# Kernel optimization log

Hardware: AMD Instinct MI355X
Metric: run time of the kernel (lower is better)

Reference implementation:

```python
import jax, jax.numpy as jnp
import numpy as np

HEADS = 8

def setup_inputs() -> dict:
    key = jax.random.key(0)
    ks = jax.random.split(key, 10)
    B, C, D, W, H = 4, 256, 12, 12, 12
    dk = C // HEADS
    return {
        "x": jax.random.normal(ks[0], (B, C, D, W, H), jnp.float32),
        "wq": jax.random.normal(ks[1], (C, C), jnp.float32) * 0.05,
        "bq": jax.random.normal(ks[2], (C,), jnp.float32) * 0.05,
        "wk": jax.random.normal(ks[3], (C, C), jnp.float32) * 0.05,
        "bk": jax.random.normal(ks[4], (C,), jnp.float32) * 0.05,
        "wv": jax.random.normal(ks[5], (C, C), jnp.float32) * 0.05,
        "bv": jax.random.normal(ks[6], (C,), jnp.float32) * 0.05,
        "rel_d": jax.random.normal(ks[7], (1, HEADS, dk, D, 1, 1), jnp.float32),
        "rel_h": jax.random.normal(ks[8], (1, HEADS, dk, 1, 1, H), jnp.float32),
        "rel_w": jax.random.normal(ks[9], (1, HEADS, dk, 1, W, 1), jnp.float32),
    }


def reference(x, wq, bq, wk, bk, wv, bv, rel_d, rel_h, rel_w):
    B, C, D, W, H = x.shape
    dk = C // HEADS
    N = D * W * H

    def proj(w, b):
        # Conv3d kernel_size=1 == per-voxel linear over channels
        y = jnp.einsum('bcdwh,oc->bodwh', x, w) + b[None, :, None, None, None]
        return y.reshape(B, HEADS, dk, N)  # [B,h,dk,N]

    q = proj(wq, bq)
    k = proj(wk, bk)
    v = proj(wv, bv)

    # content-content: q^T k -> [B,h,N,N]
    cc = jnp.einsum('bhdn,bhdm->bhnm', q, k)
    # relative-position bias: (rel_h+rel_w+rel_d) broadcasts to [1,h,dk,D,W,H]
    pos = (rel_h + rel_w + rel_d).reshape(1, HEADS, dk, N)
    # content-position: pos^T @ q -> [B,h,N,N]
    cp = jnp.einsum('bhdn,bhdm->bhnm', pos, q)

    attn = jax.nn.softmax(cc + cp, axis=-1)  # [B,h,N,N]
    # out = v @ attn^T -> [B,h,dk,N]
    out = jnp.einsum('bhdn,bhmn->bhdm', v, attn)
    return out.reshape(B, C, D, W, H)
```

## Files before the change

### kernel.cpp

```cpp
#include <hip/hip_runtime.h>
#include <math.h>

#define HEADS 8
#define DK 32
#define B_ 4
#define C_ 256
#define NVOX 1728
#define DE 64
#define XPITCH 136
#define CPITCH 36
#define LOG2E 1.44269504088896f
#define JSPLIT 2
#define ITILES 14

typedef _Float16 f16x8 __attribute__((ext_vector_type(8)));
typedef __fp16 fp16x2 __attribute__((ext_vector_type(2)));
typedef float f32x16 __attribute__((ext_vector_type(16)));

__device__ inline float h2f(short s) {
    _Float16 h = *(_Float16*)&s;
    return (float)h;
}
__device__ inline f32x16 mfma32h(f16x8 a, f16x8 b, f32x16 c) {
    return __builtin_amdgcn_mfma_f32_32x32x16_f16(a, b, c, 0, 0, 0);
}
__device__ __forceinline__ void gl_lds16(const short* g, short* l) {
    __builtin_amdgcn_global_load_lds(
        (const __attribute__((address_space(1))) unsigned int*)g,
        (__attribute__((address_space(3))) unsigned int*)l, 16, 0, 0);
}

union H8 { _Float16 h[8]; uint4 v; };
union H4 { _Float16 h[4]; uint2 v; };
union PW { fp16x2 h2; unsigned int u; };

__global__ __launch_bounds__(256)
void prep_kernel(const float* __restrict__ x,
                 const float* __restrict__ wq, const float* __restrict__ wk,
                 const float* __restrict__ wv,
                 const float* __restrict__ rel_d, const float* __restrict__ rel_h,
                 const float* __restrict__ rel_w,
                 short* __restrict__ wf, short* __restrict__ xf,
                 short* __restrict__ Qf) {
    __shared__ float tile[64][65];
    int bid = blockIdx.x;
    int t = threadIdx.x;

    if (bid < 192) {
        int idx = (bid * 256 + t) * 4;
        int m = idx >> 16;
        const float* w = (m == 0) ? wq : (m == 1) ? wk : wv;
        float4 v = *(const float4*)&w[idx & 65535];
        H4 hh;
        hh.h[0] = (_Float16)v.x; hh.h[1] = (_Float16)v.y;
        hh.h[2] = (_Float16)v.z; hh.h[3] = (_Float16)v.w;
        *(uint2*)&wf[idx] = hh.v;
    } else if (bid < 624) {
        int q = bid - 192;
        int nb = (q % 27) * 64;
        int c0 = ((q / 27) % 4) * 64;
        int b  = q / 108;
        const float* xb = x + (size_t)b * C_ * NVOX;
        for (int e = t; e < 4096; e += 256) {
            int ci = e >> 6, nl = e & 63;
            tile[ci][nl] = xb[(size_t)(c0 + ci) * NVOX + nb + nl];
        }
        __syncthreads();
        for (int e = t; e < 512; e += 256) {
            int n = e >> 3, cg = (e & 7) * 8;
            H8 hi;
            #pragma unroll
            for (int j = 0; j < 8; j++) hi.h[j] = (_Float16)tile[cg + j][n];
            *(uint4*)&xf[((size_t)b * NVOX + nb + n) * C_ + c0 + cg] = hi.v;
        }
    } else {
        int q = bid - 624;
        int nb = (q % 27) * 64;
        int h  = (q / 27) % 8;
        int b  = q / 216;
        int bh = b * HEADS + h;
        int nl = t & 63, dd0 = (t >> 6) * 8;
        int n = nb + nl;
        int di = n / 144, wi = (n / 12) % 12, hi = n % 12;
        H8 ph;
        #pragma unroll
        for (int o = 0; o < 8; o++) {
            int hd = h * DK + dd0 + o;
            ph.h[o] = (_Float16)(rel_d[hd * 12 + di] + rel_w[hd * 12 + wi] +
                                 rel_h[hd * 12 + hi]);
        }
        *(uint4*)&Qf[((size_t)bh * NVOX + n) * DE + DK + dd0] = ph.v;
    }
}

struct FS {
    union {
        short xs[64 * XPITCH];
        float cbuf[3][64][CPITCH];
    } u;
};

__global__ __launch_bounds__(384, 4)
void fproj_kernel(const short* __restrict__ xf, const short* __restrict__ wf,
                  const float* __restrict__ bq, const float* __restrict__ bk,
                  const float* __restrict__ bv,
                  short* __restrict__ Qf, short* __restrict__ Kf,
                  short* __restrict__ Vf) {
    __shared__ FS sm;
    int nb = blockIdx.x * 64, h = blockIdx.y, b = blockIdx.z;
    int bh = b * HEADS + h;
    int t = threadIdx.x;
    int w = t >> 6, l = t & 63, ln = l & 31, hv = l >> 5;
    int mat = w >> 1, nh = w & 1;

    const short* xb = xf + ((size_t)b * NVOX + nb) * C_;
    const short* wA = wf + ((size_t)mat * C_ + h * DK + ln) * C_;
    int xrow = (nh * 32 + ln) * XPITCH;

    f32x16 acc;
    #pragma unroll
    for (int r = 0; r < 16; r++) acc[r] = 0.f;

    #pragma unroll 1
    for (int ch = 0; ch < 2; ch++) {
        __syncthreads();
        for (int e = t; e < 1024; e += 384) {
            int row = e >> 4, c8 = (e & 15) * 8;
            *(uint4*)&sm.u.xs[row * XPITCH + c8] =
                *(const uint4*)&xb[row * C_ + ch * 128 + c8];
        }
        __syncthreads();
        #pragma unroll 4
        for (int ks = 0; ks < 8; ks++) {
            int kl_ = ks * 16 + hv * 8;
            f16x8 a = *(const f16x8*)&wA[ch * 128 + kl_];
            f16x8 bfr = *(const f16x8*)&sm.u.xs[xrow + kl_];
            acc = mfma32h(a, bfr, acc);
        }
    }
    __syncthreads();

    const float* bias = (mat == 0) ? bq : (mat == 1) ? bk : bv;
    int ncol = nh * 32 + ln;
    #pragma unroll
    for (int q2 = 0; q2 < 4; q2++) {
        float4 cv;
        float* cvp = (float*)&cv;
        #pragma unroll
        for (int m = 0; m < 4; m++) {
            int o_loc = 8 * q2 + 4 * hv + m;
            cvp[m] = acc[4 * q2 + m] + bias[h * DK + o_loc];
        }
        *(float4*)&sm.u.cbuf[mat][ncol][8 * q2 + 4 * hv] = cv;
    }
    __syncthreads();

    if (t < 256) {
        int n = t >> 2, ddg = (t & 3) * 8;
        H8 qh, kh;
        #pragma unroll
        for (int j = 0; j < 8; j++) {
            qh.h[j] = (_Float16)sm.u.cbuf[0][n][ddg + j];
            kh.h[j] = (_Float16)sm.u.cbuf[1][n][ddg + j];
        }
        *(uint4*)&Qf[((size_t)bh * NVOX + nb + n) * DE + ddg] = qh.v;
        *(uint4*)&Kf[((size_t)bh * NVOX + nb + n) * DK + ddg] = kh.v;
    }
    if (t < 256) {
        int d = t >> 3, ng = (t & 7) * 8;
        H8 vv;
        #pragma unroll
        for (int j = 0; j < 8; j++)
            vv.h[j] = (_Float16)sm.u.cbuf[2][ng + j][d];
        *(uint4*)&Vf[((size_t)bh * DK + d) * NVOX + nb + ng] = vv.v;
    }
}

__global__ __launch_bounds__(256, 4)
void attn_kernel(const short* __restrict__ Qf, const short* __restrict__ Kf,
                 const short* __restrict__ Vf,
                 short* __restrict__ wsO, float* __restrict__ wsM,
                 float* __restrict__ wsL) {
    __shared__ __align__(16) short Ksm[2][4096];
    __shared__ __align__(16) short Vsm[2][2048];
    int id = blockIdx.x;
    int x8 = id & 7;
    int rr = id >> 3;
    int g  = rr / 28;
    int k_ = rr - g * 28;
    int bh = g * 8 + x8;
    int it = k_ >> 1;
    int jp = k_ & 1;
    int cnt = 14 - jp;
    int t = threadIdx.x;
    int w  = t >> 6;
    int l  = t & 63;
    int ln = l & 31;
    int hv = l >> 5;
    int i_glob = it * 128 + w * 32 + ln;
    int iq = i_glob < NVOX ? i_glob : NVOX - 1;

    const short* Qp = Qf + (size_t)bh * NVOX * DE;
    const short* Kp = Kf + (size_t)bh * NVOX * DK;
    const short* Vp = Vf + (size_t)bh * DK * NVOX;

    f16x8 qf[4];
    #pragma unroll
    for (int ks = 0; ks < 4; ks++)
        qf[ks] = *(const f16x8*)&Qp[(size_t)iq * DE + ks * 16 + hv * 8];

    int jb0 = jp * 14 * 64;

    const short* gk0 = Kp + (size_t)(jb0 + (l ^ (w + 0))) * DK + (w + 0) * 8;
    const short* gk1 = Qp + (size_t)(jb0 + (l ^ (w + 4))) * DE + (w + 0) * 8;
    int vb0 = 2 * w + hv;
    const short* gv0 = Vp + (size_t)(ln ^ vb0) * NVOX + jb0 + vb0 * 8;

#define STAGE(bufp) do {                                   \
        short* kl_ = &Ksm[bufp][0];                        \
        short* vl_ = &Vsm[bufp][0];                        \
        gl_lds16(gk0, kl_ + (w + 0) * 512);                \
        gl_lds16(gk1, kl_ + (w + 4) * 512);                \
        gl_lds16(gv0, vl_ + (w + 0) * 512);                \
        gk0 += 64 * DK; gk1 += 64 * DE; gv0 += 64;         \
    } while (0)

    float mL = -INFINITY;
    float lsum = 0.f;
    f32x16 O;
    #pragma unroll
    for (int r = 0; r < 16; r++) O[r] = 0.f;

    STAGE(0);

    #pragma unroll 1
    for (int jt = 0; jt < cnt; ++jt) {
        int buf = jt & 1;
        __syncthreads();
        if (jt + 1 < cnt) STAGE(buf ^ 1);

        const short* Kb = &Ksm[buf][0];
        const short* Vb = &Vsm[buf][0];

        f32x16 sc[2];
        __builtin_amdgcn_s_setprio(1);
        #pragma unroll
        for (int js = 0; js < 2; js++) {
            f32x16 s;
            #pragma unroll
            for (int r = 0; r < 16; r++) s[r] = 0.f;
            #pragma unroll
            for (int ks = 0; ks < 4; ks++) {
                int kb = ks * 2 + hv;
                f16x8 kfr = *(const f16x8*)&Kb[kb * 512 + js * 256 + (ln ^ kb) * 8];
                s = mfma32h(kfr, qf[ks], s);
            }
            sc[js] = s;
        }
        __builtin_amdgcn_s_setprio(0);

        float m0 = fmaxf(sc[0][0], sc[1][0]);
        float m1 = fmaxf(sc[0][1], sc[1][1]);
        float m2 = fmaxf(sc[0][2], sc[1][2]);
        float m3 = fmaxf(sc[0][3], sc[1][3]);
        #pragma unroll
        for (int r = 4; r < 16; r += 4) {
            m0 = fmaxf(m0, fmaxf(sc[0][r + 0], sc[1][r + 0]));
            m1 = fmaxf(m1, fmaxf(sc[0][r + 1], sc[1][r + 1]));
            m2 = fmaxf(m2, fmaxf(sc[0][r + 2], sc[1][r + 2]));
            m3 = fmaxf(m3, fmaxf(sc[0][r + 3], sc[1][r + 3]));
        }
        float mx = fmaxf(fmaxf(m0, m1), fmaxf(m2, m3));
        mx = fmaxf(mx, __shfl_xor(mx, 32));
        float mxl = mx * LOG2E;
        if (!__all(mxl <= mL + 4.0f)) {
            float mLn = fmaxf(mL, mxl);
            float alpha = exp2f(mL - mLn);
            mL = mLn;
            lsum *= alpha;
            #pragma unroll
            for (int r = 0; r < 16; r++) O[r] *= alpha;
        }

        float ps0 = 0.f, ps1 = 0.f, ps2 = 0.f, ps3 = 0.f;
        #pragma unroll
        for (int js = 0; js < 2; js++) {
            #pragma unroll
            for (int r = 0; r < 16; r += 4) {
                float p0 = exp2f(fmaf(sc[js][r + 0], LOG2E, -mL));
                float p1 = exp2f(fmaf(sc[js][r + 1], LOG2E, -mL));
                float p2 = exp2f(fmaf(sc[js][r + 2], LOG2E, -mL));
                float p3 = exp2f(fmaf(sc[js][r + 3], LOG2E, -mL));
                sc[js][r + 0] = p0; sc[js][r + 1] = p1;
                sc[js][r + 2] = p2; sc[js][r + 3] = p3;
                ps0 += p0; ps1 += p1; ps2 += p2; ps3 += p3;
            }
        }
        float ps = (ps0 + ps1) + (ps2 + ps3);
        ps += __shfl_xor(ps, 32);
        lsum += ps;

        __builtin_amdgcn_s_setprio(1);
        #pragma unroll
        for (int ks = 0; ks < 4; ks++) {
            int js = ks >> 1, u8 = (ks & 1) * 8;
            PW a0p, a1p, b0p, b1p;
            a0p.h2 = __builtin_amdgcn_cvt_pkrtz(sc[js][u8 + 0], sc[js][u8 + 1]);
            a1p.h2 = __builtin_amdgcn_cvt_pkrtz(sc[js][u8 + 2], sc[js][u8 + 3]);
            b0p.h2 = __builtin_amdgcn_cvt_pkrtz(sc[js][u8 + 4], sc[js][u8 + 5]);
            b1p.h2 = __builtin_amdgcn_cvt_pkrtz(sc[js][u8 + 6], sc[js][u8 + 7]);
            auto r0 = __builtin_amdgcn_permlane32_swap(a0p.u, b0p.u, false, false);
            auto r1 = __builtin_amdgcn_permlane32_swap(a1p.u, b1p.u, false, false);
            union { unsigned int w4[4]; f16x8 f; } pb;
            pb.w4[0] = r0[0]; pb.w4[1] = r1[0];
            pb.w4[2] = r0[1]; pb.w4[3] = r1[1];
            int vb = ks * 2 + hv;
            f16x8 va = *(const f16x8*)&Vb[vb * 256 + (ln ^ vb) * 8];
            O = mfma32h(va, pb.f, O);
        }
        __builtin_amdgcn_s_setprio(0);
    }
#undef STAGE

    if (i_glob < NVOX) {
        short* Op = wsO + ((size_t)jp * (B_ * HEADS) + bh) * DK * NVOX;
        #pragma unroll
        for (int r = 0; r < 16; r++) {
            int d = (r & 3) + 8 * (r >> 2) + 4 * hv;
            _Float16 oh = (_Float16)O[r];
            Op[(size_t)d * NVOX + i_glob] = *(short*)&oh;
        }
        if (hv == 0) {
            size_t mo = ((size_t)jp * (B_ * HEADS) + bh) * NVOX + i_glob;
            wsM[mo] = mL;
            wsL[mo] = lsum;
        }
    }
}

__global__ void combine_kernel(const short* __restrict__ wsO,
                               const float* __restrict__ wsM,
                               const float* __restrict__ wsL,
                               float* __restrict__ out) {
    int idx = (blockIdx.x * 256 + threadIdx.x) * 4;
    int i = idx % NVOX;
    int bh = (idx / NVOX) >> 5;
    const size_t oh = (size_t)B_ * HEADS * DK * NVOX;
    const size_t mh = (size_t)B_ * HEADS * NVOX;
    size_t mo = (size_t)bh * NVOX + i;
    float4 m0 = *(const float4*)&wsM[mo];
    float4 m1 = *(const float4*)&wsM[mh + mo];
    float4 l0 = *(const float4*)&wsL[mo];
    float4 l1 = *(const float4*)&wsL[mh + mo];
    uint2 o0u = *(const uint2*)&wsO[idx];
    uint2 o1u = *(const uint2*)&wsO[oh + idx];
    const short* o0s = (const short*)&o0u;
    const short* o1s = (const short*)&o1u;
    const float* m0p = (const float*)&m0; const float* m1p = (const float*)&m1;
    const float* l0p = (const float*)&l0; const float* l1p = (const float*)&l1;
    float4 res;
    float* rp = (float*)&res;
    #pragma unroll
    for (int j = 0; j < 4; j++) {
        float m = fmaxf(m0p[j], m1p[j]);
        float a0 = exp2f(m0p[j] - m);
        float a1 = exp2f(m1p[j] - m);
        rp[j] = (a0 * h2f(o0s[j]) + a1 * h2f(o1s[j])) /
                (a0 * l0p[j] + a1 * l1p[j]);
    }
    *(float4*)&out[idx] = res;
}

extern "C" void kernel_launch(void* const* d_in, const int* in_sizes, int n_in,
                              void* d_out, int out_size, void* d_ws, size_t ws_size,
                              hipStream_t stream) {
    const float* x     = (const float*)d_in[0];
    const float* wq    = (const float*)d_in[1];
    const float* bq    = (const float*)d_in[2];
    const float* wk    = (const float*)d_in[3];
    const float* bk    = (const float*)d_in[4];
    const float* wv    = (const float*)d_in[5];
    const float* bv    = (const float*)d_in[6];
    const float* rel_d = (const float*)d_in[7];
    const float* rel_h = (const float*)d_in[8];
    const float* rel_w = (const float*)d_in[9];
    float* out = (float*)d_out;

    size_t qksz = (size_t)B_ * HEADS * NVOX * DE;
    size_t vsz  = (size_t)B_ * HEADS * DK * NVOX;
    short* Qf  = (short*)d_ws;
    short* Kf  = Qf + qksz;
    short* Vf  = Kf + vsz;
    short* wf  = Vf + vsz;
    short* wsO = wf + (size_t)3 * C_ * C_;
    float* wsM = (float*)(wsO + 2 * vsz);
    float* wsL = wsM + 2 * (size_t)B_ * HEADS * NVOX;
    short* xf  = wsO;

    prep_kernel<<<dim3(1488), dim3(256), 0, stream>>>(
        x, wq, wk, wv, rel_d, rel_h, rel_w, wf, xf, Qf);
    fproj_kernel<<<dim3(NVOX / 64, HEADS, B_), dim3(384), 0, stream>>>(
        xf, wf, bq, bk, bv, Qf, Kf, Vf);
    attn_kernel<<<dim3(ITILES * JSPLIT * HEADS * B_), dim3(256), 0, stream>>>(
        Qf, Kf, Vf, wsO, wsM, wsL);
    combine_kernel<<<dim3((int)(vsz / 1024)), dim3(256), 0, stream>>>(wsO, wsM, wsL, out);
}
```

Baseline: 153.8 us.

## Drop key-split and combine kernel; normalize output directly in attention kernel

Removes the two-way split over key tiles and the separate combine kernel: each attention block now iterates over all 27 key tiles and writes the normalized fp32 output directly. This eliminates the fp16 partial-output and max/sum workspace traffic and one kernel launch. In exchange the attention grid halves, so each block runs twice as long with fewer concurrent blocks to hide latency.

```diff
diff --git a/kernel.cpp b/kernel.cpp
--- a/kernel.cpp
+++ b/kernel.cpp
@@ -10,7 +10,7 @@
 #define XPITCH 136
 #define CPITCH 36
 #define LOG2E 1.44269504088896f
-#define JSPLIT 2
+#define NJT 27
 #define ITILES 14
 
 typedef _Float16 f16x8 __attribute__((ext_vector_type(8)));
@@ -178,20 +178,15 @@
 
 __global__ __launch_bounds__(256, 4)
 void attn_kernel(const short* __restrict__ Qf, const short* __restrict__ Kf,
-                 const short* __restrict__ Vf,
-                 short* __restrict__ wsO, float* __restrict__ wsM,
-                 float* __restrict__ wsL) {
+                 const short* __restrict__ Vf, float* __restrict__ out) {
     __shared__ __align__(16) short Ksm[2][4096];
     __shared__ __align__(16) short Vsm[2][2048];
     int id = blockIdx.x;
     int x8 = id & 7;
     int rr = id >> 3;
-    int g  = rr / 28;
-    int k_ = rr - g * 28;
+    int g  = rr / 14;
+    int it = rr - g * 14;
     int bh = g * 8 + x8;
-    int it = k_ >> 1;
-    int jp = k_ & 1;
-    int cnt = 14 - jp;
     int t = threadIdx.x;
     int w  = t >> 6;
     int l  = t & 63;
@@ -209,12 +204,10 @@
     for (int ks = 0; ks < 4; ks++)
         qf[ks] = *(const f16x8*)&Qp[(size_t)iq * DE + ks * 16 + hv * 8];
 
-    int jb0 = jp * 14 * 64;
-
-    const short* gk0 = Kp + (size_t)(jb0 + (l ^ (w + 0))) * DK + (w + 0) * 8;
-    const short* gk1 = Qp + (size_t)(jb0 + (l ^ (w + 4))) * DE + (w + 0) * 8;
+    const short* gk0 = Kp + (size_t)(l ^ (w + 0)) * DK + (w + 0) * 8;
+    const short* gk1 = Qp + (size_t)(l ^ (w + 4)) * DE + (w + 0) * 8;
     int vb0 = 2 * w + hv;
-    const short* gv0 = Vp + (size_t)(ln ^ vb0) * NVOX + jb0 + vb0 * 8;
+    const short* gv0 = Vp + (size_t)(ln ^ vb0) * NVOX + vb0 * 8;
 
 #define STAGE(bufp) do {                                   \
         short* kl_ = &Ksm[bufp][0];                        \
@@ -234,10 +227,10 @@
     STAGE(0);
 
     #pragma unroll 1
-    for (int jt = 0; jt < cnt; ++jt) {
+    for (int jt = 0; jt < NJT; ++jt) {
         int buf = jt & 1;
         __syncthreads();
-        if (jt + 1 < cnt) STAGE(buf ^ 1);
+        if (jt + 1 < NJT) STAGE(buf ^ 1);
 
         const short* Kb = &Ksm[buf][0];
         const short* Vb = &Vsm[buf][0];
@@ -323,52 +316,14 @@
 #undef STAGE
 
     if (i_glob < NVOX) {
-        short* Op = wsO + ((size_t)jp * (B_ * HEADS) + bh) * DK * NVOX;
+        float inv = 1.0f / lsum;
+        float* Op = out + (size_t)bh * DK * NVOX;
         #pragma unroll
         for (int r = 0; r < 16; r++) {
             int d = (r & 3) + 8 * (r >> 2) + 4 * hv;
-            _Float16 oh = (_Float16)O[r];
-            Op[(size_t)d * NVOX + i_glob] = *(short*)&oh;
-        }
-        if (hv == 0) {
-            size_t mo = ((size_t)jp * (B_ * HEADS) + bh) * NVOX + i_glob;
-            wsM[mo] = mL;
-            wsL[mo] = lsum;
-        }
-    }
-}
-
-__global__ void combine_kernel(const short* __restrict__ wsO,
-                               const float* __restrict__ wsM,
-                               const float* __restrict__ wsL,
-                               float* __restrict__ out) {
-    int idx = (blockIdx.x * 256 + threadIdx.x) * 4;
-    int i = idx % NVOX;
-    int bh = (idx / NVOX) >> 5;
-    const size_t oh = (size_t)B_ * HEADS * DK * NVOX;
-    const size_t mh = (size_t)B_ * HEADS * NVOX;
-    size_t mo = (size_t)bh * NVOX + i;
-    float4 m0 = *(const float4*)&wsM[mo];
-    float4 m1 = *(const float4*)&wsM[mh + mo];
-    float4 l0 = *(const float4*)&wsL[mo];
-    float4 l1 = *(const float4*)&wsL[mh + mo];
-    uint2 o0u = *(const uint2*)&wsO[idx];
-    uint2 o1u = *(const uint2*)&wsO[oh + idx];
-    const short* o0s = (const short*)&o0u;
-    const short* o1s = (const short*)&o1u;
-    const float* m0p = (const float*)&m0; const float* m1p = (const float*)&m1;
-    const float* l0p = (const float*)&l0; const float* l1p = (const float*)&l1;
-    float4 res;
-    float* rp = (float*)&res;
-    #pragma unroll
-    for (int j = 0; j < 4; j++) {
-        float m = fmaxf(m0p[j], m1p[j]);
-        float a0 = exp2f(m0p[j] - m);
-        float a1 = exp2f(m1p[j] - m);
-        rp[j] = (a0 * h2f(o0s[j]) + a1 * h2f(o1s[j])) /
-                (a0 * l0p[j] + a1 * l1p[j]);
-    }
-    *(float4*)&out[idx] = res;
+            Op[(size_t)d * NVOX + i_glob] = O[r] * inv;
+        }
+    }
 }
 
 extern "C" void kernel_launch(void* const* d_in, const int* in_sizes, int n_in,
@@ -392,16 +347,12 @@
     short* Kf  = Qf + qksz;
     short* Vf  = Kf + vsz;
     short* wf  = Vf + vsz;
-    short* wsO = wf + (size_t)3 * C_ * C_;
-    float* wsM = (float*)(wsO + 2 * vsz);
-    float* wsL = wsM + 2 * (size_t)B_ * HEADS * NVOX;
-    short* xf  = wsO;
+    short* xf  = wf + (size_t)3 * C_ * C_;
 
     prep_kernel<<<dim3(1488), dim3(256), 0, stream>>>(
         x, wq, wk, wv, rel_d, rel_h, rel_w, wf, xf, Qf);
     fproj_kernel<<<dim3(NVOX / 64, HEADS, B_), dim3(384), 0, stream>>>(
         xf, wf, bq, bk, bv, Qf, Kf, Vf);
-    attn_kernel<<<dim3(ITILES * JSPLIT * HEADS * B_), dim3(256), 0, stream>>>(
-        Qf, Kf, Vf, wsO, wsM, wsL);
-    combine_kernel<<<dim3((int)(vsz / 1024)), dim3(256), 0, stream>>>(wsO, wsM, wsL, out);
-}
+    attn_kernel<<<dim3(ITILES * HEADS * B_), dim3(256), 0, stream>>>(
+        Qf, Kf, Vf, out);
+}
```

Measured after the change: 154.5 us. Within noise of the previous version (+0.4%).
